# Kernel tuning notes

Measured on AMD Instinct MI355X. Metric: run time of the kernel, lower is better.

Reference implementation:

```python
import jax, jax.numpy as jnp
import numpy as np

B_, L_, D_ = 2, 1024, 2048
E_, N_, R_, K_ = 4096, 16, 128, 4
EPS = 1e-5


def setup_inputs() -> dict:
    key = jax.random.key(0)
    ks = jax.random.split(key, 12)
    s = lambda i, shape, scale=0.02: jax.random.normal(ks[i], shape, jnp.float32) * scale
    # dt bias init as in the module: inv_dt = dt + log(-expm1(-dt)), dt ~ logU[1e-3, 0.1]
    dt = jnp.exp(jax.random.uniform(ks[10], (E_,)) * (np.log(0.1) - np.log(0.001)) + np.log(0.001))
    inv_dt = dt + jnp.log(-jnp.expm1(-dt))
    return {
        'resid': jax.random.normal(ks[0], (B_, L_, D_), jnp.float32),
        'norm_w': jnp.ones((D_,), jnp.float32),
        'skip_w': s(1, (E_, D_)),
        'in_w': s(2, (E_, D_)),
        'conv_w': s(3, (E_, K_), 0.2),
        'conv_b': jnp.zeros((E_,), jnp.float32),
        'wd1': s(4, (R_, E_)),
        'wd2': s(5, (E_, R_), R_ ** -0.5),
        'wd2_b': inv_dt,
        'wB': s(6, (N_, E_)),
        'wC': s(7, (N_, E_)),
        'A_log': jnp.log(jnp.broadcast_to(jnp.arange(1, N_ + 1, dtype=jnp.float32), (E_, N_))),
        'W_D': jnp.ones((E_,), jnp.float32),
        'out_w': s(8, (D_, E_)),
    }


def _forward(resid, norm_w, skip_w, in_w, conv_w, conv_b, wd1, wd2, wd2_b,
             wB, wC, A_log, W_D, out_w):
    B, L, D = resid.shape
    E, K = conv_w.shape
    N = A_log.shape[1]
    # RMSNorm
    rn = resid * jax.lax.rsqrt(jnp.mean(resid * resid, -1, keepdims=True) + EPS) * norm_w
    skip = rn @ skip_w.T                       # [B,L,E] gate branch (z)
    x_in = rn @ in_w.T                         # [B,L,E]
    # depthwise causal conv1d (pad left K-1, truncate to L), then SiLU
    xp = jnp.pad(x_in, ((0, 0), (K - 1, 0), (0, 0)))
    conv = conv_b + sum(xp[:, k:k + L, :] * conv_w[:, k] for k in range(K))
    x = jax.nn.silu(conv)                      # [B,L,E] ssm input
    # low-rank delta, input-dependent B/C
    delta = jax.nn.softplus((x @ wd1.T) @ wd2.T + wd2_b)   # [B,L,E]
    A = -jnp.exp(A_log)                        # [E,N]
    Bm = x @ wB.T                              # [B,L,N]
    Cm = x @ wC.T                              # [B,L,N]

    def step(h, inp):
        d_l, b_l, c_l, x_l = inp               # [B,E],[B,N],[B,N],[B,E]
        h = jnp.exp(d_l[:, :, None] * A) * h + (d_l * x_l)[:, :, None] * b_l[:, None, :]
        y_l = jnp.einsum('ben,bn->be', h, c_l)
        return h, y_l

    h0 = jnp.zeros((B, E, N), resid.dtype)
    xs = (delta.transpose(1, 0, 2), Bm.transpose(1, 0, 2),
          Cm.transpose(1, 0, 2), x.transpose(1, 0, 2))
    _, ys = jax.lax.scan(step, h0, xs)         # ys: [L,B,E]
    y = ys.transpose(1, 0, 2) + x * W_D        # skip connection via D
    y = y * jax.nn.silu(skip)                  # gating
    return resid + y @ out_w.T                 # out_proj + residual


def reference(resid, norm_w, skip_w, in_w, conv_w, conv_b, wd1, wd2, wd2_b,
              wB, wC, A_log, W_D, out_w):
    return _forward(resid, norm_w, skip_w, in_w, conv_w, conv_b, wd1, wd2,
                    wd2_b, wB, wC, A_log, W_D, out_w)
```

## Files before the change

### kernel.cpp

```cpp
#include <hip/hip_runtime.h>
#include <stdint.h>

#define NB 2
#define NL 1024
#define ND 2048
#define NE 4096
#define NN 16
#define NR 128
#define NKC 4
#define NBL (NB*NL)
#define EPSV 1e-5f

typedef __attribute__((ext_vector_type(4))) float f32x4;
typedef __attribute__((ext_vector_type(8))) short short8;
typedef __attribute__((ext_vector_type(8))) unsigned short ushort8;
typedef __attribute__((ext_vector_type(4))) unsigned short ushort4_t;

__device__ __forceinline__ unsigned short f2bf(float f) {
  union { float f; unsigned u; } v; v.f = f;
  unsigned r = v.u + 0x7FFFu + ((v.u >> 16) & 1u);
  return (unsigned short)(r >> 16);
}

__device__ __forceinline__ void load_lds16(const void* g, void* l) {
  __builtin_amdgcn_global_load_lds((const __attribute__((address_space(1))) void*)g,
                                   (__attribute__((address_space(3))) void*)l,
                                   16, 0, 0);
}

template<int CTRL>
__device__ __forceinline__ float dpp_mov(float v) {
  return __int_as_float(__builtin_amdgcn_update_dpp(
      0, __float_as_int(v), CTRL, 0xF, 0xF, true));
}

__global__ void rmsnorm_kernel(const float* __restrict__ resid,
                               const float* __restrict__ nw,
                               unsigned short* __restrict__ rn) {
  int row = blockIdx.x;
  int tid = threadIdx.x;
  const float* r = resid + (size_t)row * ND;
  f32x4 v0 = *(const f32x4*)(r + tid * 8);
  f32x4 v1 = *(const f32x4*)(r + tid * 8 + 4);
  float vals[8];
#pragma unroll
  for (int i = 0; i < 4; ++i) { vals[i] = v0[i]; vals[4 + i] = v1[i]; }
  float ss = 0.f;
#pragma unroll
  for (int i = 0; i < 8; ++i) ss += vals[i] * vals[i];
  for (int o = 32; o > 0; o >>= 1) ss += __shfl_down(ss, o);
  __shared__ float ps[4];
  if ((tid & 63) == 0) ps[tid >> 6] = ss;
  __syncthreads();
  float tot = ps[0] + ps[1] + ps[2] + ps[3];
  float scale = rsqrtf(tot / (float)ND + EPSV);
  ushort8 o8;
#pragma unroll
  for (int i = 0; i < 8; ++i) o8[i] = f2bf(vals[i] * scale * nw[tid * 8 + i]);
  *(ushort8*)(rn + (size_t)row * ND + tid * 8) = o8;
}

__global__ void cast_bf16_kernel(const float* __restrict__ in,
                                 unsigned short* __restrict__ out, int n8) {
  int i = blockIdx.x * blockDim.x + threadIdx.x;
  if (i >= n8) return;
  f32x4 a = *(const f32x4*)(in + (size_t)i * 8);
  f32x4 b = *(const f32x4*)(in + (size_t)i * 8 + 4);
  ushort8 o;
#pragma unroll
  for (int j = 0; j < 4; ++j) { o[j] = f2bf(a[j]); o[4 + j] = f2bf(b[j]); }
  *(ushort8*)(out + (size_t)i * 8) = o;
}

__global__ void build_wcat_kernel(const float* __restrict__ wd1,
                                  const float* __restrict__ wB,
                                  const float* __restrict__ wC,
                                  unsigned short* __restrict__ out) {
  int i = blockIdx.x * blockDim.x + threadIdx.x;
  if (i >= 256 * NE / 8) return;
  int col8 = i & (NE / 8 - 1);
  int row = i >> 9;
  const float* src = nullptr; int srow = 0;
  if (row < 128)      { src = wd1; srow = row; }
  else if (row < 144) { src = wB;  srow = row - 128; }
  else if (row < 160) { src = wC;  srow = row - 144; }
  ushort8 o;
  if (src) {
    f32x4 a = *(const f32x4*)(src + (size_t)srow * NE + col8 * 8);
    f32x4 b = *(const f32x4*)(src + (size_t)srow * NE + col8 * 8 + 4);
#pragma unroll
    for (int j = 0; j < 4; ++j) { o[j] = f2bf(a[j]); o[4 + j] = f2bf(b[j]); }
  } else {
#pragma unroll
    for (int j = 0; j < 8; ++j) o[j] = 0;
  }
  *(ushort8*)(out + (size_t)row * NE + col8 * 8) = o;
}

template<int MODE>
__global__ __launch_bounds__(256)
void gemm_bt(const unsigned short* __restrict__ A,
             const unsigned short* __restrict__ B,
             float* __restrict__ C,
             int M, int N, int K, int ksteps_per_z,
             const float* __restrict__ bias,
             const float* __restrict__ add) {
  __shared__ unsigned short As[128 * 32];
  __shared__ unsigned short Bs[128 * 32];
  int tid = threadIdx.x;
  int w = tid >> 6, lane = tid & 63;
  int m0 = blockIdx.y * 128, n0 = blockIdx.x * 128;
  int kz0 = blockIdx.z * ksteps_per_z * 32;
  if (MODE == 0) C += (size_t)blockIdx.z * M * N;

  f32x4 zero = {0.f, 0.f, 0.f, 0.f};
  f32x4 acc[4][4];
#pragma unroll
  for (int i = 0; i < 4; ++i)
#pragma unroll
    for (int j = 0; j < 4; ++j) acc[i][j] = zero;

  int wm = w >> 1, wn = w & 1;
  int lr = lane & 15, kg = lane >> 4;

  int fe0 = (w)*512 + lane * 8;
  int fe1 = (4 + w) * 512 + lane * 8;
  int r0 = fe0 >> 5, c0 = fe0 & 31;
  int r1 = fe1 >> 5, c1 = fe1 & 31;
  const unsigned short* Ag0 = A + (size_t)(m0 + r0) * K + c0;
  const unsigned short* Ag1 = A + (size_t)(m0 + r1) * K + c1;
  const unsigned short* Bg0 = B + (size_t)(n0 + r0) * K + c0;
  const unsigned short* Bg1 = B + (size_t)(n0 + r1) * K + c1;
  unsigned short* Al0 = As + (w) * 512;
  unsigned short* Al1 = As + (4 + w) * 512;
  unsigned short* Bl0 = Bs + (w) * 512;
  unsigned short* Bl1 = Bs + (4 + w) * 512;

  for (int ks = 0; ks < ksteps_per_z; ++ks) {
    int kk = kz0 + ks * 32;
    __syncthreads();
    load_lds16(Ag0 + kk, Al0);
    load_lds16(Ag1 + kk, Al1);
    load_lds16(Bg0 + kk, Bl0);
    load_lds16(Bg1 + kk, Bl1);
    asm volatile("s_waitcnt vmcnt(0)" ::: "memory");
    __syncthreads();
    short8 a[4], b[4];
#pragma unroll
    for (int i = 0; i < 4; ++i)
      a[i] = *(const short8*)&As[(wm * 64 + i * 16 + lr) * 32 + kg * 8];
#pragma unroll
    for (int j = 0; j < 4; ++j)
      b[j] = *(const short8*)&Bs[(wn * 64 + j * 16 + lr) * 32 + kg * 8];
#pragma unroll
    for (int i = 0; i < 4; ++i)
#pragma unroll
      for (int j = 0; j < 4; ++j)
        acc[i][j] = __builtin_amdgcn_mfma_f32_16x16x32_bf16(a[i], b[j], acc[i][j], 0, 0, 0);
  }

#pragma unroll
  for (int i = 0; i < 4; ++i) {
#pragma unroll
    for (int j = 0; j < 4; ++j) {
      int rbase = m0 + wm * 64 + i * 16 + kg * 4;
      int col = n0 + wn * 64 + j * 16 + lr;
#pragma unroll
      for (int r = 0; r < 4; ++r) {
        float v = acc[i][j][r];
        size_t idx = (size_t)(rbase + r) * N + col;
        if (MODE == 0) {
          C[idx] = v;
        } else if (MODE == 1) {
          float t = v + bias[col];
          C[idx] = (t > 20.f) ? t : log1pf(__expf(t));
        } else {
          C[idx] = v + add[idx];
        }
      }
    }
  }
}

__global__ void conv_silu_kernel(const float* __restrict__ xin,
                                 const float* __restrict__ cw,
                                 const float* __restrict__ cb,
                                 float* __restrict__ x,
                                 unsigned short* __restrict__ xbf) {
  size_t idx = (size_t)blockIdx.x * blockDim.x + threadIdx.x;
  if (idx >= (size_t)NB * NL * NE) return;
  int e = (int)(idx & (NE - 1));
  int l = (int)((idx >> 12) & (NL - 1));
  float acc = cb[e];
#pragma unroll
  for (int k = 0; k < NKC; ++k) {
    int ls = l - 3 + k;
    if (ls >= 0) acc += xin[idx + (size_t)(k - 3) * NE] * cw[e * 4 + k];
  }
  float s = acc / (1.f + __expf(-acc));
  x[idx] = s;
  xbf[idx] = f2bf(s);
}

__global__ void reduce_tcat_kernel(const float* __restrict__ part,
                                   unsigned short* __restrict__ tbf,
                                   float* __restrict__ Bm,
                                   float* __restrict__ Cm) {
  int idx = blockIdx.x * blockDim.x + threadIdx.x;
  if (idx >= NBL * 160) return;
  int m = idx / 160, c = idx - m * 160;
  float s = 0.f;
#pragma unroll
  for (int z = 0; z < 8; ++z) s += part[(size_t)z * NBL * 256 + (size_t)m * 256 + c];
  if (c < 128) tbf[m * 128 + c] = f2bf(s);
  else if (c < 144) Bm[m * 16 + (c - 128)] = s;
  else Cm[m * 16 + (c - 144)] = s;
}

#define SCAN_T 64
__global__ __launch_bounds__(256)
void scan_kernel(const float* __restrict__ delta,
                 const float* __restrict__ x,
                 const float* __restrict__ Bm,
                 const float* __restrict__ Cm,
                 const float* __restrict__ skip,
                 const float* __restrict__ A_log,
                 const float* __restrict__ W_D,
                 unsigned short* __restrict__ yg) {
  __shared__ float dl[2][SCAN_T][16];
  __shared__ float xl[2][SCAN_T][16];
  __shared__ float sl[2][SCAN_T][16];
  __shared__ float Bl[2][SCAN_T][16];
  __shared__ float Cl[2][SCAN_T][16];
  __shared__ float yl[SCAN_T][16];
  int tid = threadIdx.x;
  int n = tid & 15, el = tid >> 4;
  int w = tid >> 6, lane = tid & 63;
  int e0 = blockIdx.x * 16;
  int b = blockIdx.y;
  int e = e0 + el;
  float Aen = -__expf(A_log[e * 16 + n]);
  float wd = W_D[e];
  float h = 0.f;

  const float* gd = delta + (size_t)b * NL * NE + e0;
  const float* gx = x + (size_t)b * NL * NE + e0;
  const float* gs = skip + (size_t)b * NL * NE + e0;
  const float* gB = Bm + (size_t)b * NL * 16;
  const float* gC = Cm + (size_t)b * NL * 16;

  int srow = w * 16 + (lane >> 2);
  int scol = (lane & 3) * 4;

  auto stage = [&](int buf, int c) {
    int l0 = c * SCAN_T;
    load_lds16(gd + (size_t)(l0 + srow) * NE + scol, &dl[buf][w * 16][0]);
    load_lds16(gx + (size_t)(l0 + srow) * NE + scol, &xl[buf][w * 16][0]);
    load_lds16(gs + (size_t)(l0 + srow) * NE + scol, &sl[buf][w * 16][0]);
    load_lds16(gB + (size_t)l0 * 16 + w * 256 + lane * 4, &Bl[buf][w * 16][0]);
    load_lds16(gC + (size_t)l0 * 16 + w * 256 + lane * 4, &Cl[buf][w * 16][0]);
  };

  stage(0, 0);
  const int nch = NL / SCAN_T;
  for (int c = 0; c < nch; ++c) {
    int cur = c & 1;
    if (c + 1 < nch) {
      stage(cur ^ 1, c + 1);
      asm volatile("s_waitcnt vmcnt(5)" ::: "memory");
    } else {
      asm volatile("s_waitcnt vmcnt(0)" ::: "memory");
    }
    __syncthreads();
    int l0 = c * SCAN_T;
#pragma unroll 4
    for (int t = 0; t < SCAN_T; ++t) {
      float dc = dl[cur][t][el];
      float xc = xl[cur][t][el];
      float Bc = Bl[cur][t][n];
      float Cc = Cl[cur][t][n];
      h = __expf(dc * Aen) * h + (dc * xc) * Bc;
      float p = h * Cc;
      p += dpp_mov<0xB1>(p);
      p += dpp_mov<0x4E>(p);
      p += dpp_mov<0x141>(p);
      p += dpp_mov<0x140>(p);
      if (n == 0) yl[t][el] = p + xc * wd;
    }
    __syncthreads();
    {
      int t = tid >> 2, part = tid & 3;
      f32x4 yv = *(const f32x4*)&yl[t][part * 4];
      f32x4 sv = *(const f32x4*)&sl[cur][t][part * 4];
      ushort4_t o;
#pragma unroll
      for (int j = 0; j < 4; ++j) {
        float g = sv[j] / (1.f + __expf(-sv[j]));
        o[j] = f2bf(yv[j] * g);
      }
      *(ushort4_t*)(yg + (size_t)(b * NL + l0 + t) * NE + e0 + part * 4) = o;
    }
    __syncthreads();
  }
}

extern "C" void kernel_launch(void* const* d_in, const int* in_sizes, int n_in,
                              void* d_out, int out_size, void* d_ws, size_t ws_size,
                              hipStream_t stream) {
  const float* resid  = (const float*)d_in[0];
  const float* norm_w = (const float*)d_in[1];
  const float* skip_w = (const float*)d_in[2];
  const float* in_w   = (const float*)d_in[3];
  const float* conv_w = (const float*)d_in[4];
  const float* conv_b = (const float*)d_in[5];
  const float* wd1    = (const float*)d_in[6];
  const float* wd2    = (const float*)d_in[7];
  const float* wd2_b  = (const float*)d_in[8];
  const float* wB     = (const float*)d_in[9];
  const float* wC     = (const float*)d_in[10];
  const float* A_log  = (const float*)d_in[11];
  const float* W_D    = (const float*)d_in[12];
  const float* out_w  = (const float*)d_in[13];
  float* out = (float*)d_out;

  char* ws = (char*)d_ws;
  size_t off = 0;
  auto alloc = [&](size_t bytes) -> void* {
    void* p = ws + off;
    off += (bytes + 255) & ~(size_t)255;
    return p;
  };
  unsigned short* rn_bf    = (unsigned short*)alloc((size_t)NBL * ND * 2);
  unsigned short* wskip_bf = (unsigned short*)alloc((size_t)NE * ND * 2);
  unsigned short* win_bf   = (unsigned short*)alloc((size_t)NE * ND * 2);
  unsigned short* wout_bf  = (unsigned short*)alloc((size_t)ND * NE * 2);
  unsigned short* wd2_bf   = (unsigned short*)alloc((size_t)NE * NR * 2);
  unsigned short* wcat_bf  = (unsigned short*)alloc((size_t)256 * NE * 2);
  float* skip_f            = (float*)alloc((size_t)NBL * NE * 4);
  float* xin_f             = (float*)alloc((size_t)NBL * NE * 4);
  float* x_f               = (float*)alloc((size_t)NBL * NE * 4);
  unsigned short* x_bf     = (unsigned short*)alloc((size_t)NBL * NE * 2);
  float* part_f            = (float*)alloc((size_t)8 * NBL * 256 * 4);
  unsigned short* t_bf     = (unsigned short*)alloc((size_t)NBL * NR * 2);
  float* Bm_f              = (float*)alloc((size_t)NBL * 16 * 4);
  float* Cm_f              = (float*)alloc((size_t)NBL * 16 * 4);
  unsigned short* yg_bf    = (unsigned short*)alloc((size_t)NBL * NE * 2);
  float* delta_f = xin_f;
  (void)ws_size; (void)in_sizes; (void)n_in; (void)out_size;

  rmsnorm_kernel<<<dim3(NBL), dim3(256), 0, stream>>>(resid, norm_w, rn_bf);

  cast_bf16_kernel<<<dim3((NE * ND / 8 + 255) / 256), dim3(256), 0, stream>>>(skip_w, wskip_bf, NE * ND / 8);
  cast_bf16_kernel<<<dim3((NE * ND / 8 + 255) / 256), dim3(256), 0, stream>>>(in_w, win_bf, NE * ND / 8);
  cast_bf16_kernel<<<dim3((ND * NE / 8 + 255) / 256), dim3(256), 0, stream>>>(out_w, wout_bf, ND * NE / 8);
  cast_bf16_kernel<<<dim3((NE * NR / 8 + 255) / 256), dim3(256), 0, stream>>>(wd2, wd2_bf, NE * NR / 8);
  build_wcat_kernel<<<dim3(256 * NE / 8 / 256), dim3(256), 0, stream>>>(wd1, wB, wC, wcat_bf);

  gemm_bt<0><<<dim3(NE / 128, NBL / 128, 1), dim3(256), 0, stream>>>(
      rn_bf, wskip_bf, skip_f, NBL, NE, ND, ND / 32, nullptr, nullptr);
  gemm_bt<0><<<dim3(NE / 128, NBL / 128, 1), dim3(256), 0, stream>>>(
      rn_bf, win_bf, xin_f, NBL, NE, ND, ND / 32, nullptr, nullptr);

  conv_silu_kernel<<<dim3((int)(((size_t)NB * NL * NE) / 256)), dim3(256), 0, stream>>>(
      xin_f, conv_w, conv_b, x_f, x_bf);

  gemm_bt<0><<<dim3(256 / 128, NBL / 128, 8), dim3(256), 0, stream>>>(
      x_bf, wcat_bf, part_f, NBL, 256, NE, (NE / 32) / 8, nullptr, nullptr);
  reduce_tcat_kernel<<<dim3((NBL * 160 + 255) / 256), dim3(256), 0, stream>>>(
      part_f, t_bf, Bm_f, Cm_f);

  gemm_bt<1><<<dim3(NE / 128, NBL / 128, 1), dim3(256), 0, stream>>>(
      t_bf, wd2_bf, delta_f, NBL, NE, NR, NR / 32, wd2_b, nullptr);

  scan_kernel<<<dim3(NE / 16, NB), dim3(256), 0, stream>>>(
      delta_f, x_f, Bm_f, Cm_f, skip_f, A_log, W_D, yg_bf);

  gemm_bt<2><<<dim3(ND / 128, NBL / 128, 1), dim3(256), 0, stream>>>(
      yg_bf, wout_bf, out, NBL, ND, NE, NE / 32, nullptr, resid);
}
```

Baseline: 479.2 us.

## Merge skip/in projections into one GEMM and shrink scan inputs to bf16

Concatenates the skip and in projection weights so a single GEMM produces both, with SiLU of the gate fused into its epilogue. The scan now reads delta and x as bf16, B and C interleaved in one buffer, and the precomputed gate, and it uses a raw exp2 with a prescaled A. The fp32 x buffer is dropped, and delta is stored in bf16 in space reused from the weight buffer. This cuts memory traffic and kernel launches, at the cost of bf16 rounding on delta and x inside the recurrence.

```diff
diff --git a/kernel.cpp b/kernel.cpp
--- a/kernel.cpp
+++ b/kernel.cpp
@@ -20,6 +20,10 @@
   union { float f; unsigned u; } v; v.f = f;
   unsigned r = v.u + 0x7FFFu + ((v.u >> 16) & 1u);
   return (unsigned short)(r >> 16);
+}
+
+__device__ __forceinline__ float bf2f(unsigned short u) {
+  union { unsigned u; float f; } v; v.u = (unsigned)u << 16; return v.f;
 }
 
 __device__ __forceinline__ void load_lds16(const void* g, void* l) {
@@ -173,39 +177,40 @@
           C[idx] = v;
         } else if (MODE == 1) {
           float t = v + bias[col];
-          C[idx] = (t > 20.f) ? t : log1pf(__expf(t));
+          ((unsigned short*)C)[idx] = f2bf((t > 20.f) ? t : log1pf(__expf(t)));
+        } else if (MODE == 2) {
+          C[idx] = v + add[idx];
         } else {
-          C[idx] = v + add[idx];
+          if (n0 < 4096) C[idx] = v / (1.f + __expf(-v));
+          else           C[idx] = v;
         }
       }
     }
   }
 }
 
-__global__ void conv_silu_kernel(const float* __restrict__ xin,
+__global__ void conv_silu_kernel(const float* __restrict__ cat,
                                  const float* __restrict__ cw,
                                  const float* __restrict__ cb,
-                                 float* __restrict__ x,
                                  unsigned short* __restrict__ xbf) {
   size_t idx = (size_t)blockIdx.x * blockDim.x + threadIdx.x;
   if (idx >= (size_t)NB * NL * NE) return;
   int e = (int)(idx & (NE - 1));
-  int l = (int)((idx >> 12) & (NL - 1));
+  int r = (int)(idx >> 12);
+  int l = r & (NL - 1);
   float acc = cb[e];
 #pragma unroll
   for (int k = 0; k < NKC; ++k) {
     int ls = l - 3 + k;
-    if (ls >= 0) acc += xin[idx + (size_t)(k - 3) * NE] * cw[e * 4 + k];
+    if (ls >= 0) acc += cat[(size_t)(r - 3 + k) * 8192 + 4096 + e] * cw[e * 4 + k];
   }
   float s = acc / (1.f + __expf(-acc));
-  x[idx] = s;
   xbf[idx] = f2bf(s);
 }
 
 __global__ void reduce_tcat_kernel(const float* __restrict__ part,
                                    unsigned short* __restrict__ tbf,
-                                   float* __restrict__ Bm,
-                                   float* __restrict__ Cm) {
+                                   float* __restrict__ bc) {
   int idx = blockIdx.x * blockDim.x + threadIdx.x;
   if (idx >= NBL * 160) return;
   int m = idx / 160, c = idx - m * 160;
@@ -213,25 +218,22 @@
 #pragma unroll
   for (int z = 0; z < 8; ++z) s += part[(size_t)z * NBL * 256 + (size_t)m * 256 + c];
   if (c < 128) tbf[m * 128 + c] = f2bf(s);
-  else if (c < 144) Bm[m * 16 + (c - 128)] = s;
-  else Cm[m * 16 + (c - 144)] = s;
+  else if (c < 144) bc[m * 32 + (c - 128)] = s;
+  else bc[m * 32 + 16 + (c - 144)] = s;
 }
 
 #define SCAN_T 64
 __global__ __launch_bounds__(256)
-void scan_kernel(const float* __restrict__ delta,
-                 const float* __restrict__ x,
-                 const float* __restrict__ Bm,
-                 const float* __restrict__ Cm,
-                 const float* __restrict__ skip,
+void scan_kernel(const unsigned short* __restrict__ delta_bf,
+                 const unsigned short* __restrict__ x_bf,
+                 const float* __restrict__ bc,
+                 const float* __restrict__ gcat,
                  const float* __restrict__ A_log,
                  const float* __restrict__ W_D,
                  unsigned short* __restrict__ yg) {
-  __shared__ float dl[2][SCAN_T][16];
-  __shared__ float xl[2][SCAN_T][16];
-  __shared__ float sl[2][SCAN_T][16];
-  __shared__ float Bl[2][SCAN_T][16];
-  __shared__ float Cl[2][SCAN_T][16];
+  __shared__ unsigned short dxl[2][SCAN_T][2][16];
+  __shared__ float gl[2][SCAN_T][16];
+  __shared__ float BCl[2][SCAN_T][32];
   __shared__ float yl[SCAN_T][16];
   int tid = threadIdx.x;
   int n = tid & 15, el = tid >> 4;
@@ -239,26 +241,29 @@
   int e0 = blockIdx.x * 16;
   int b = blockIdx.y;
   int e = e0 + el;
-  float Aen = -__expf(A_log[e * 16 + n]);
+  float A2 = -__expf(A_log[e * 16 + n]) * 1.44269504f;
   float wd = W_D[e];
   float h = 0.f;
 
-  const float* gd = delta + (size_t)b * NL * NE + e0;
-  const float* gx = x + (size_t)b * NL * NE + e0;
-  const float* gs = skip + (size_t)b * NL * NE + e0;
-  const float* gB = Bm + (size_t)b * NL * 16;
-  const float* gC = Cm + (size_t)b * NL * 16;
-
-  int srow = w * 16 + (lane >> 2);
-  int scol = (lane & 3) * 4;
+  const unsigned short* gdl = delta_bf + (size_t)b * NL * NE + e0;
+  const unsigned short* gx  = x_bf + (size_t)b * NL * NE + e0;
+  const float* gg  = gcat + (size_t)b * NL * 8192 + e0;
+  const float* gBC = bc + (size_t)b * NL * 32;
+
+  const unsigned short* dxsrc = ((lane >> 1) & 1) ? gx : gdl;
+  int dxrow = w * 16 + (lane >> 2);
+  int dxcol = (lane & 1) * 8;
+  int grow = w * 16 + (lane >> 2);
+  int gcol = (lane & 3) * 4;
+  int bcrow = lane >> 3;
+  int bccol = (lane & 7) * 4;
 
   auto stage = [&](int buf, int c) {
     int l0 = c * SCAN_T;
-    load_lds16(gd + (size_t)(l0 + srow) * NE + scol, &dl[buf][w * 16][0]);
-    load_lds16(gx + (size_t)(l0 + srow) * NE + scol, &xl[buf][w * 16][0]);
-    load_lds16(gs + (size_t)(l0 + srow) * NE + scol, &sl[buf][w * 16][0]);
-    load_lds16(gB + (size_t)l0 * 16 + w * 256 + lane * 4, &Bl[buf][w * 16][0]);
-    load_lds16(gC + (size_t)l0 * 16 + w * 256 + lane * 4, &Cl[buf][w * 16][0]);
+    load_lds16(dxsrc + (size_t)(l0 + dxrow) * NE + dxcol, &dxl[buf][w * 16][0][0]);
+    load_lds16(gg + (size_t)(l0 + grow) * 8192 + gcol, &gl[buf][w * 16][0]);
+    load_lds16(gBC + (size_t)(l0 + w * 16 + bcrow) * 32 + bccol, &BCl[buf][w * 16][0]);
+    load_lds16(gBC + (size_t)(l0 + w * 16 + 8 + bcrow) * 32 + bccol, &BCl[buf][w * 16 + 8][0]);
   };
 
   stage(0, 0);
@@ -267,19 +272,21 @@
     int cur = c & 1;
     if (c + 1 < nch) {
       stage(cur ^ 1, c + 1);
-      asm volatile("s_waitcnt vmcnt(5)" ::: "memory");
+      asm volatile("s_waitcnt vmcnt(4)" ::: "memory");
     } else {
       asm volatile("s_waitcnt vmcnt(0)" ::: "memory");
     }
     __syncthreads();
     int l0 = c * SCAN_T;
-#pragma unroll 4
+#pragma unroll 8
     for (int t = 0; t < SCAN_T; ++t) {
-      float dc = dl[cur][t][el];
-      float xc = xl[cur][t][el];
-      float Bc = Bl[cur][t][n];
-      float Cc = Cl[cur][t][n];
-      h = __expf(dc * Aen) * h + (dc * xc) * Bc;
+      float dc = bf2f(dxl[cur][t][0][el]);
+      float xc = bf2f(dxl[cur][t][1][el]);
+      float Bc = BCl[cur][t][n];
+      float Cc = BCl[cur][t][16 + n];
+      float a = dc * A2, ed;
+      asm("v_exp_f32 %0, %1" : "=v"(ed) : "v"(a));
+      h = ed * h + (dc * xc) * Bc;
       float p = h * Cc;
       p += dpp_mov<0xB1>(p);
       p += dpp_mov<0x4E>(p);
@@ -291,13 +298,10 @@
     {
       int t = tid >> 2, part = tid & 3;
       f32x4 yv = *(const f32x4*)&yl[t][part * 4];
-      f32x4 sv = *(const f32x4*)&sl[cur][t][part * 4];
+      f32x4 gv = *(const f32x4*)&gl[cur][t][part * 4];
       ushort4_t o;
 #pragma unroll
-      for (int j = 0; j < 4; ++j) {
-        float g = sv[j] / (1.f + __expf(-sv[j]));
-        o[j] = f2bf(yv[j] * g);
-      }
+      for (int j = 0; j < 4; ++j) o[j] = f2bf(yv[j] * gv[j]);
       *(ushort4_t*)(yg + (size_t)(b * NL + l0 + t) * NE + e0 + part * 4) = o;
     }
     __syncthreads();
@@ -330,50 +334,44 @@
     off += (bytes + 255) & ~(size_t)255;
     return p;
   };
-  unsigned short* rn_bf    = (unsigned short*)alloc((size_t)NBL * ND * 2);
-  unsigned short* wskip_bf = (unsigned short*)alloc((size_t)NE * ND * 2);
-  unsigned short* win_bf   = (unsigned short*)alloc((size_t)NE * ND * 2);
-  unsigned short* wout_bf  = (unsigned short*)alloc((size_t)ND * NE * 2);
-  unsigned short* wd2_bf   = (unsigned short*)alloc((size_t)NE * NR * 2);
-  unsigned short* wcat_bf  = (unsigned short*)alloc((size_t)256 * NE * 2);
-  float* skip_f            = (float*)alloc((size_t)NBL * NE * 4);
-  float* xin_f             = (float*)alloc((size_t)NBL * NE * 4);
-  float* x_f               = (float*)alloc((size_t)NBL * NE * 4);
-  unsigned short* x_bf     = (unsigned short*)alloc((size_t)NBL * NE * 2);
-  float* part_f            = (float*)alloc((size_t)8 * NBL * 256 * 4);
-  unsigned short* t_bf     = (unsigned short*)alloc((size_t)NBL * NR * 2);
-  float* Bm_f              = (float*)alloc((size_t)NBL * 16 * 4);
-  float* Cm_f              = (float*)alloc((size_t)NBL * 16 * 4);
-  unsigned short* yg_bf    = (unsigned short*)alloc((size_t)NBL * NE * 2);
-  float* delta_f = xin_f;
+  unsigned short* rn_bf      = (unsigned short*)alloc((size_t)NBL * ND * 2);
+  unsigned short* wskipin_bf = (unsigned short*)alloc((size_t)2 * NE * ND * 2);
+  unsigned short* wout_bf    = (unsigned short*)alloc((size_t)ND * NE * 2);
+  unsigned short* wd2_bf     = (unsigned short*)alloc((size_t)NE * NR * 2);
+  unsigned short* wcat_bf    = (unsigned short*)alloc((size_t)256 * NE * 2);
+  float* cat_f               = (float*)alloc((size_t)NBL * 8192 * 4);
+  unsigned short* x_bf       = (unsigned short*)alloc((size_t)NBL * NE * 2);
+  float* part_f              = (float*)alloc((size_t)8 * NBL * 256 * 4);
+  unsigned short* t_bf       = (unsigned short*)alloc((size_t)NBL * NR * 2);
+  float* bc_f                = (float*)alloc((size_t)NBL * 32 * 4);
+  unsigned short* yg_bf      = (unsigned short*)alloc((size_t)NBL * NE * 2);
+  unsigned short* delta_bf = wskipin_bf;
   (void)ws_size; (void)in_sizes; (void)n_in; (void)out_size;
 
   rmsnorm_kernel<<<dim3(NBL), dim3(256), 0, stream>>>(resid, norm_w, rn_bf);
 
-  cast_bf16_kernel<<<dim3((NE * ND / 8 + 255) / 256), dim3(256), 0, stream>>>(skip_w, wskip_bf, NE * ND / 8);
-  cast_bf16_kernel<<<dim3((NE * ND / 8 + 255) / 256), dim3(256), 0, stream>>>(in_w, win_bf, NE * ND / 8);
+  cast_bf16_kernel<<<dim3((NE * ND / 8 + 255) / 256), dim3(256), 0, stream>>>(skip_w, wskipin_bf, NE * ND / 8);
+  cast_bf16_kernel<<<dim3((NE * ND / 8 + 255) / 256), dim3(256), 0, stream>>>(in_w, wskipin_bf + (size_t)NE * ND, NE * ND / 8);
   cast_bf16_kernel<<<dim3((ND * NE / 8 + 255) / 256), dim3(256), 0, stream>>>(out_w, wout_bf, ND * NE / 8);
   cast_bf16_kernel<<<dim3((NE * NR / 8 + 255) / 256), dim3(256), 0, stream>>>(wd2, wd2_bf, NE * NR / 8);
   build_wcat_kernel<<<dim3(256 * NE / 8 / 256), dim3(256), 0, stream>>>(wd1, wB, wC, wcat_bf);
 
-  gemm_bt<0><<<dim3(NE / 128, NBL / 128, 1), dim3(256), 0, stream>>>(
-      rn_bf, wskip_bf, skip_f, NBL, NE, ND, ND / 32, nullptr, nullptr);
-  gemm_bt<0><<<dim3(NE / 128, NBL / 128, 1), dim3(256), 0, stream>>>(
-      rn_bf, win_bf, xin_f, NBL, NE, ND, ND / 32, nullptr, nullptr);
+  gemm_bt<3><<<dim3(8192 / 128, NBL / 128, 1), dim3(256), 0, stream>>>(
+      rn_bf, wskipin_bf, cat_f, NBL, 8192, ND, ND / 32, nullptr, nullptr);
 
   conv_silu_kernel<<<dim3((int)(((size_t)NB * NL * NE) / 256)), dim3(256), 0, stream>>>(
-      xin_f, conv_w, conv_b, x_f, x_bf);
+      cat_f, conv_w, conv_b, x_bf);
 
   gemm_bt<0><<<dim3(256 / 128, NBL / 128, 8), dim3(256), 0, stream>>>(
       x_bf, wcat_bf, part_f, NBL, 256, NE, (NE / 32) / 8, nullptr, nullptr);
   reduce_tcat_kernel<<<dim3((NBL * 160 + 255) / 256), dim3(256), 0, stream>>>(
-      part_f, t_bf, Bm_f, Cm_f);
+      part_f, t_bf, bc_f);
 
   gemm_bt<1><<<dim3(NE / 128, NBL / 128, 1), dim3(256), 0, stream>>>(
-      t_bf, wd2_bf, delta_f, NBL, NE, NR, NR / 32, wd2_b, nullptr);
+      t_bf, wd2_bf, (float*)delta_bf, NBL, NE, NR, NR / 32, wd2_b, nullptr);
 
   scan_kernel<<<dim3(NE / 16, NB), dim3(256), 0, stream>>>(
-      delta_f, x_f, Bm_f, Cm_f, skip_f, A_log, W_D, yg_bf);
+      delta_bf, x_bf, bc_f, cat_f, A_log, W_D, yg_bf);
 
   gemm_bt<2><<<dim3(ND / 128, NBL / 128, 1), dim3(256), 0, stream>>>(
       yg_bf, wout_bf, out, NBL, ND, NE, NE / 32, nullptr, resid);
```

Result: faster. 458.1 us (-4.4%).
